# Kernel tuning notes

Hardware: AMD Instinct MI355X
Metric: run time of the kernel (lower is better)

## Reference

```python
import jax, jax.numpy as jnp
import numpy as np

N_NODES = 50000
N_EDGES = 1600000
D = 64  # per-node feature dim for h1 and h2


def setup_inputs() -> dict:
    key = jax.random.key(0)
    ks = jax.random.split(key, 8)
    h1 = jax.random.normal(ks[0], (N_NODES, D), dtype=jnp.float32)
    h2 = jax.random.normal(ks[1], (N_NODES, D), dtype=jnp.float32)
    src = jax.random.randint(ks[2], (N_EDGES,), 0, N_NODES)
    dst = jax.random.randint(ks[3], (N_EDGES,), 0, N_NODES)
    # MLP params: layer_sizes = [256, 128, 128, 1]
    def glorot(k, fan_in, fan_out):
        lim = (6.0 / (fan_in + fan_out)) ** 0.5
        return jax.random.uniform(k, (fan_in, fan_out), jnp.float32, -lim, lim)
    W0 = glorot(ks[4], 4 * D, 128)
    W1 = glorot(ks[5], 128, 128)
    W2 = glorot(ks[6], 128, 1)
    b0 = jnp.zeros((128,), jnp.float32)
    b1 = jnp.zeros((128,), jnp.float32)
    b2 = jnp.zeros((1,), jnp.float32)
    return {"h1": h1, "h2": h2, "src": src, "dst": dst,
            "W0": W0, "b0": b0, "W1": W1, "b1": b1, "W2": W2, "b2": b2}


def reference(h1, h2, src, dst, W0, b0, W1, b1, W2, b2):
    # Edge-wise gather of src/dst node features, concat -> MLP (eval mode: dropout=identity).
    h = jnp.concatenate([h1[src], h1[dst], h2[src], h2[dst]], axis=1)  # [E, 4D]
    h = h @ W0 + b0
    h = jax.nn.relu(h) @ W1 + b1
    h = jax.nn.relu(h) @ W2 + b2
    return h  # [E, out_features]
```

## Files before the change

### kernel.cpp

```cpp
#include <hip/hip_runtime.h>
#include <hip/hip_bf16.h>
#include <stdint.h>


typedef __attribute__((ext_vector_type(8))) __bf16 bf16x8;
typedef __attribute__((ext_vector_type(4))) __bf16 bf16x4;
typedef __attribute__((ext_vector_type(4))) float  floatx4;

__device__ inline floatx4 mfma16x16x32(bf16x8 a, bf16x8 b, floatx4 c) {
  return __builtin_amdgcn_mfma_f32_16x16x32_bf16(a, b, c, 0, 0, 0);
}

__device__ inline void bar_lds() {
  asm volatile("s_waitcnt lgkmcnt(0)" ::: "memory");
  __builtin_amdgcn_s_barrier();
}

__global__ void cvt_w_kernel(const float* __restrict__ W0, const float* __restrict__ W1,
                             __bf16* __restrict__ W1T, __bf16* __restrict__ W0uT,
                             __bf16* __restrict__ W0wT) {
  const int t = blockIdx.x * 256 + threadIdx.x;
  if (t < 16384) {
    const int n = t >> 7, k = t & 127;
    W1T[t] = (__bf16)W1[k * 128 + n];
  } else if (t < 32768) {
    const int t2 = t - 16384;
    const int n = t2 >> 7, k2 = t2 & 127;
    const int row = (k2 < 64) ? k2 : 64 + k2;
    W0uT[t2] = (__bf16)W0[row * 128 + n];
  } else {
    const int t3 = t - 32768;
    const int n = t3 >> 7, k2 = t3 & 127;
    const int row = (k2 < 64) ? 64 + k2 : 128 + k2;
    W0wT[t3] = (__bf16)W0[row * 128 + n];
  }
}

__global__ __launch_bounds__(256, 2)
void node_uw_kernel(const float* __restrict__ h1, const float* __restrict__ h2,
                    const __bf16* __restrict__ W0uT, const __bf16* __restrict__ W0wT,
                    const float* __restrict__ b0,
                    __bf16* __restrict__ uTab, __bf16* __restrict__ wTab, int nNodes) {
  __shared__ char sN[64 * 256];
  const int tid = threadIdx.x;
  const int base = blockIdx.x * 64;

  {
    const int r = tid >> 2, q = tid & 3;
    const int node = base + r;
    const int swz = (r & 7) << 4;
#pragma unroll
    for (int ii = 0; ii < 4; ++ii) {
      const int c = q * 4 + ii;
      bf16x8 v;
      if (node < nNodes) {
        const float* sp = (c < 8) ? (h1 + (size_t)node * 64 + c * 8)
                                  : (h2 + (size_t)node * 64 + (c - 8) * 8);
        const float4 x = reinterpret_cast<const float4*>(sp)[0];
        const float4 y = reinterpret_cast<const float4*>(sp)[1];
        v[0] = (__bf16)x.x; v[1] = (__bf16)x.y; v[2] = (__bf16)x.z; v[3] = (__bf16)x.w;
        v[4] = (__bf16)y.x; v[5] = (__bf16)y.y; v[6] = (__bf16)y.z; v[7] = (__bf16)y.w;
      } else {
#pragma unroll
        for (int k = 0; k < 8; ++k) v[k] = (__bf16)0.f;
      }
      *reinterpret_cast<bf16x8*>(sN + r * 256 + ((c * 16) ^ swz)) = v;
    }
  }
  __syncthreads();

  const int lane = tid & 63;
  const int l15 = lane & 15;
  const int hi = lane >> 4;
  const int hi16 = hi * 16;
  const int wvU = __builtin_amdgcn_readfirstlane(tid >> 6);

  float b0c[2][4];
#pragma unroll
  for (int nt = 0; nt < 2; ++nt)
#pragma unroll
    for (int r = 0; r < 4; ++r) b0c[nt][r] = b0[wvU * 32 + nt * 16 + hi * 4 + r];

#pragma unroll
  for (int pass = 0; pass < 2; ++pass) {
    const __bf16* Wt = pass ? W0wT : W0uT;
    __bf16* Tab = pass ? wTab : uTab;
    const bf16x8* wp = reinterpret_cast<const bf16x8*>(Wt);
    bf16x8 wf[4][2];
#pragma unroll
    for (int kk = 0; kk < 4; ++kk) {
      wf[kk][0] = wp[(wvU * 32 + l15) * 16 + kk * 4 + hi];
      wf[kk][1] = wp[(wvU * 32 + 16 + l15) * 16 + kk * 4 + hi];
    }
    floatx4 acc[4][2];
#pragma unroll
    for (int mt = 0; mt < 4; ++mt) { acc[mt][0] = (floatx4)0.f; acc[mt][1] = (floatx4)0.f; }
#pragma unroll
    for (int kk = 0; kk < 4; ++kk) {
#pragma unroll
      for (int mt = 0; mt < 4; ++mt) {
        const int row = mt * 16 + l15;
        const bf16x8 a = *reinterpret_cast<const bf16x8*>(
            sN + row * 256 + ((kk * 64 + hi16) ^ ((row & 7) << 4)));
        acc[mt][0] = mfma16x16x32(wf[kk][0], a, acc[mt][0]);
        acc[mt][1] = mfma16x16x32(wf[kk][1], a, acc[mt][1]);
      }
    }
#pragma unroll
    for (int mt = 0; mt < 4; ++mt) {
      const int node = base + mt * 16 + l15;
      if (node < nNodes) {
#pragma unroll
        for (int nt = 0; nt < 2; ++nt) {
          bf16x4 pk;
#pragma unroll
          for (int r = 0; r < 4; ++r) {
            const float v = acc[mt][nt][r] + (pass ? 0.f : b0c[nt][r]);
            pk[r] = (__bf16)v;
          }
          *reinterpret_cast<bf16x4*>(Tab + (size_t)node * 128 + wvU * 32 + nt * 16 +
                                     hi * 4) = pk;
        }
      }
    }
  }
}

__global__ __launch_bounds__(256, 2)
void edge_uw_kernel(const __bf16* __restrict__ uTab, const __bf16* __restrict__ wTab,
                    const int* __restrict__ srcI, const int* __restrict__ dstI,
                    const __bf16* __restrict__ W1T, const float* __restrict__ b1,
                    const float* __restrict__ W2, const float* __restrict__ b2,
                    float* __restrict__ out, int E, int nTiles) {
  __shared__ char sUW[2 * 64 * 512];
  __shared__ char sH[64 * 256];

  const int tid = threadIdx.x;
  const int lane = tid & 63;
  const int l15 = lane & 15;
  const int hi = lane >> 4;
  const int hi16 = hi * 16;
  const int wvU = __builtin_amdgcn_readfirstlane(tid >> 6);
  const int wv16 = wvU * 16;
  const int wvByte = wvU * 8192;

  const int lhalf = lane >> 5;
  const int p31 = lane & 31;
  const int half = (p31 >> 4) & 1;
  const int* gIdxTab = half ? dstI : srcI;
  const __bf16* gTab = half ? wTab : uTab;

  bf16x8 w1f[4][2];
  const bf16x8* w1p = reinterpret_cast<const bf16x8*>(W1T);
#pragma unroll
  for (int kk = 0; kk < 4; ++kk) {
    w1f[kk][0] = w1p[(wvU * 32 + l15) * 16 + kk * 4 + hi];
    w1f[kk][1] = w1p[(wvU * 32 + 16 + l15) * 16 + kk * 4 + hi];
  }
  float b1c[2][4], w2c[2][4];
#pragma unroll
  for (int nt = 0; nt < 2; ++nt)
#pragma unroll
    for (int r = 0; r < 4; ++r) {
      const int n = wvU * 32 + nt * 16 + hi * 4 + r;
      b1c[nt][r] = b1[n];
      w2c[nt][r] = W2[n];
    }
  const float b2v = b2[0];

  const int tstride = gridDim.x;

  auto loadIdx = [&](int (&d)[8], int tt2) {
    const bool valid = tt2 < nTiles;
#pragma unroll
    for (int i = 0; i < 8; ++i) {
      const int eLoc = wv16 + i * 2 + lhalf;
      const int ge = tt2 * 64 + eLoc;
      d[i] = (valid && ge < E) ? gIdxTab[ge] : 0;
    }
  };

  auto issueGather = [&](int nb, const int (&idx8)[8]) {
#pragma unroll
    for (int i = 0; i < 8; ++i) {
      const int eLoc = wv16 + i * 2 + lhalf;
      const int wc = (p31 & 8) | ((p31 & 7) ^ (eLoc & 7));
      const __bf16* g = gTab + (size_t)idx8[i] * 128 + (wc & 15) * 8;
      char* l = sUW + nb * 32768 + wvByte + i * 1024;
      __builtin_amdgcn_global_load_lds(
          (const __attribute__((address_space(1))) void*)g,
          (__attribute__((address_space(3))) void*)l, 16, 0, 0);
    }
  };

  const int tile0 = blockIdx.x;
  int idxA[8], idxB[8];
  loadIdx(idxA, tile0);
  issueGather(0, idxA);
  loadIdx(idxB, tile0 + tstride);
  int cur = 0;

  for (int tt = tile0; tt < nTiles; tt += tstride) {
    __syncthreads();

    if (tt + tstride < nTiles) issueGather(cur ^ 1, idxB);
    loadIdx(idxA, tt + 2 * tstride);

    const char* sUWc = sUW + cur * 32768;

    {
      const int aR = wv16 + (lane >> 2);
      const int acq = lane & 3;
      const int aswz = (aR & 7) << 4;
      const char* rowU = sUWc + aR * 512;
      char* rowH = sH + aR * 256;
#pragma unroll
      for (int ii = 0; ii < 4; ++ii) {
        const int c = acq * 4 + ii;
        const int off = (c * 16) ^ aswz;
        const bf16x8 uu = *reinterpret_cast<const bf16x8*>(rowU + off);
        const bf16x8 ww = *reinterpret_cast<const bf16x8*>(rowU + 256 + off);
        bf16x8 hh;
#pragma unroll
        for (int k = 0; k < 8; ++k)
          hh[k] = (__bf16)fmaxf((float)uu[k] + (float)ww[k], 0.0f);
        *reinterpret_cast<bf16x8*>(rowH + off) = hh;
      }
    }
    bar_lds();

    floatx4 acc2T[4][2];
#pragma unroll
    for (int mt = 0; mt < 4; ++mt) { acc2T[mt][0] = (floatx4)0.f; acc2T[mt][1] = (floatx4)0.f; }
#pragma unroll
    for (int kk = 0; kk < 4; ++kk) {
#pragma unroll
      for (int mt = 0; mt < 4; ++mt) {
        const int row = mt * 16 + l15;
        const bf16x8 a = *reinterpret_cast<const bf16x8*>(
            sH + row * 256 + ((kk * 64 + hi16) ^ ((row & 7) << 4)));
        acc2T[mt][0] = mfma16x16x32(w1f[kk][0], a, acc2T[mt][0]);
        acc2T[mt][1] = mfma16x16x32(w1f[kk][1], a, acc2T[mt][1]);
      }
    }

    float* sRedF = (float*)sUWc;
#pragma unroll
    for (int mt = 0; mt < 4; ++mt) {
      float pp = 0.f;
#pragma unroll
      for (int nt = 0; nt < 2; ++nt)
#pragma unroll
        for (int r = 0; r < 4; ++r)
          pp += fmaxf(acc2T[mt][nt][r] + b1c[nt][r], 0.0f) * w2c[nt][r];
      pp += __shfl_xor(pp, 16);
      pp += __shfl_xor(pp, 32);
      if (lane < 16) sRedF[wvU * 64 + mt * 16 + l15] = pp;
    }
    bar_lds();

    if (tid < 64) {
      const int ge = tt * 64 + tid;
      if (ge < E) {
        out[ge] = sRedF[tid] + sRedF[64 + tid] + sRedF[128 + tid] +
                  sRedF[192 + tid] + b2v;
      }
    }

#pragma unroll
    for (int i = 0; i < 8; ++i) idxB[i] = idxA[i];
    cur ^= 1;
  }
}

__global__ void edge_mlp_fallback(const float* __restrict__ h1, const float* __restrict__ h2,
                                  const int* __restrict__ src, const int* __restrict__ dst,
                                  const float* __restrict__ W0, const float* __restrict__ b0,
                                  const float* __restrict__ W1, const float* __restrict__ b1,
                                  const float* __restrict__ W2, const float* __restrict__ b2,
                                  float* __restrict__ out, int E) {
  __shared__ float sa[256];
  __shared__ float sh[128];
  __shared__ float sr[128];
  const int e = blockIdx.x;
  if (e >= E) return;
  const int t = threadIdx.x;
  const int is = src[e], id = dst[e];
  if (t < 64) { sa[t] = h1[is * 64 + t]; sa[128 + t] = h2[is * 64 + t]; }
  else { const int u = t - 64; sa[64 + u] = h1[id * 64 + u]; sa[192 + u] = h2[id * 64 + u]; }
  __syncthreads();
  float a0 = b0[t];
  for (int k = 0; k < 256; ++k) a0 += sa[k] * W0[k * 128 + t];
  sh[t] = fmaxf(a0, 0.f);
  __syncthreads();
  float a1 = b1[t];
  for (int k = 0; k < 128; ++k) a1 += sh[k] * W1[k * 128 + t];
  sr[t] = fmaxf(a1, 0.f) * W2[t];
  __syncthreads();
  if (t == 0) {
    float s = b2[0];
    for (int k = 0; k < 128; ++k) s += sr[k];
    out[e] = s;
  }
}

extern "C" void kernel_launch(void* const* d_in, const int* in_sizes, int n_in,
                              void* d_out, int out_size, void* d_ws, size_t ws_size,
                              hipStream_t stream) {
  const float* h1 = (const float*)d_in[0];
  const float* h2 = (const float*)d_in[1];
  const int* src = (const int*)d_in[2];
  const int* dst = (const int*)d_in[3];
  const float* W0 = (const float*)d_in[4];
  const float* b0 = (const float*)d_in[5];
  const float* W1 = (const float*)d_in[6];
  const float* b1 = (const float*)d_in[7];
  const float* W2 = (const float*)d_in[8];
  const float* b2 = (const float*)d_in[9];
  float* out = (float*)d_out;

  const int D = 64;
  const int nNodes = in_sizes[0] / D;
  const int E = in_sizes[2];

  char* ws = (char*)d_ws;
  __bf16* W1T = (__bf16*)(ws);
  __bf16* W0uT = (__bf16*)(ws + 32768);
  __bf16* W0wT = (__bf16*)(ws + 65536);
  const size_t tabBytes = (size_t)nNodes * 128 * sizeof(__bf16);
  __bf16* uTab = (__bf16*)(ws + 98304);
  __bf16* wTab = (__bf16*)(ws + 98304 + tabBytes);
  const bool useFast = ws_size >= 98304 + 2 * tabBytes;

  if (!useFast) {
    edge_mlp_fallback<<<dim3(E), dim3(128), 0, stream>>>(
        h1, h2, src, dst, W0, b0, W1, b1, W2, b2, out, E);
    return;
  }

  cvt_w_kernel<<<dim3(192), dim3(256), 0, stream>>>(W0, W1, W1T, W0uT, W0wT);
  node_uw_kernel<<<dim3((nNodes + 63) / 64), dim3(256), 0, stream>>>(
      h1, h2, W0uT, W0wT, b0, uTab, wTab, nNodes);

  const int nTiles = (E + 63) / 64;
  const int grid = nTiles < 1024 ? nTiles : 1024;
  edge_uw_kernel<<<dim3(grid), dim3(256), 0, stream>>>(
      uTab, wTab, src, dst, W1T, b1, W2, b2, out, E, nTiles);
}
```

Before: 168.1 us.

## Split edge tile across 8 waves with 2x4 M/N wave grid

The edge kernel now runs 512 threads per block, with 8 waves arranged as 2 row-groups by 4 column-groups over each 64-edge tile. Each wave gathers half as many rows, holds half as many MFMA accumulators, and the cross-wave reduction is stored interleaved so one float4 read produces each output. The grid is halved to 512 blocks to keep total waves roughly constant. The aim is more waves in flight per tile to hide gather latency. The cost is more wave-level synchronisation per tile and W1 fragments being duplicated across the two row-group waves.

```diff
diff --git a/kernel.cpp b/kernel.cpp
--- a/kernel.cpp
+++ b/kernel.cpp
@@ -126,7 +126,7 @@
   }
 }
 
-__global__ __launch_bounds__(256, 2)
+__global__ __launch_bounds__(512, 2)
 void edge_uw_kernel(const __bf16* __restrict__ uTab, const __bf16* __restrict__ wTab,
                     const int* __restrict__ srcI, const int* __restrict__ dstI,
                     const __bf16* __restrict__ W1T, const float* __restrict__ b1,
@@ -141,8 +141,9 @@
   const int hi = lane >> 4;
   const int hi16 = hi * 16;
   const int wvU = __builtin_amdgcn_readfirstlane(tid >> 6);
-  const int wv16 = wvU * 16;
-  const int wvByte = wvU * 8192;
+  const int wm = wvU >> 2;
+  const int wn = wvU & 3;
+  const int wvByte = wvU * 4096;
 
   const int lhalf = lane >> 5;
   const int p31 = lane & 31;
@@ -154,15 +155,15 @@
   const bf16x8* w1p = reinterpret_cast<const bf16x8*>(W1T);
 #pragma unroll
   for (int kk = 0; kk < 4; ++kk) {
-    w1f[kk][0] = w1p[(wvU * 32 + l15) * 16 + kk * 4 + hi];
-    w1f[kk][1] = w1p[(wvU * 32 + 16 + l15) * 16 + kk * 4 + hi];
+    w1f[kk][0] = w1p[(wn * 32 + l15) * 16 + kk * 4 + hi];
+    w1f[kk][1] = w1p[(wn * 32 + 16 + l15) * 16 + kk * 4 + hi];
   }
   float b1c[2][4], w2c[2][4];
 #pragma unroll
   for (int nt = 0; nt < 2; ++nt)
 #pragma unroll
     for (int r = 0; r < 4; ++r) {
-      const int n = wvU * 32 + nt * 16 + hi * 4 + r;
+      const int n = wn * 32 + nt * 16 + hi * 4 + r;
       b1c[nt][r] = b1[n];
       w2c[nt][r] = W2[n];
     }
@@ -170,22 +171,22 @@
 
   const int tstride = gridDim.x;
 
-  auto loadIdx = [&](int (&d)[8], int tt2) {
+  auto loadIdx = [&](int (&d)[4], int tt2) {
     const bool valid = tt2 < nTiles;
 #pragma unroll
-    for (int i = 0; i < 8; ++i) {
-      const int eLoc = wv16 + i * 2 + lhalf;
+    for (int i = 0; i < 4; ++i) {
+      const int eLoc = wvU * 8 + i * 2 + lhalf;
       const int ge = tt2 * 64 + eLoc;
       d[i] = (valid && ge < E) ? gIdxTab[ge] : 0;
     }
   };
 
-  auto issueGather = [&](int nb, const int (&idx8)[8]) {
-#pragma unroll
-    for (int i = 0; i < 8; ++i) {
-      const int eLoc = wv16 + i * 2 + lhalf;
+  auto issueGather = [&](int nb, const int (&idx4)[4]) {
+#pragma unroll
+    for (int i = 0; i < 4; ++i) {
+      const int eLoc = wvU * 8 + i * 2 + lhalf;
       const int wc = (p31 & 8) | ((p31 & 7) ^ (eLoc & 7));
-      const __bf16* g = gTab + (size_t)idx8[i] * 128 + (wc & 15) * 8;
+      const __bf16* g = gTab + (size_t)idx4[i] * 128 + wc * 8;
       char* l = sUW + nb * 32768 + wvByte + i * 1024;
       __builtin_amdgcn_global_load_lds(
           (const __attribute__((address_space(1))) void*)g,
@@ -194,7 +195,7 @@
   };
 
   const int tile0 = blockIdx.x;
-  int idxA[8], idxB[8];
+  int idxA[4], idxB[4];
   loadIdx(idxA, tile0);
   issueGather(0, idxA);
   loadIdx(idxB, tile0 + tstride);
@@ -209,14 +210,14 @@
     const char* sUWc = sUW + cur * 32768;
 
     {
-      const int aR = wv16 + (lane >> 2);
-      const int acq = lane & 3;
+      const int aR = tid >> 3;
+      const int q = tid & 7;
       const int aswz = (aR & 7) << 4;
       const char* rowU = sUWc + aR * 512;
       char* rowH = sH + aR * 256;
 #pragma unroll
-      for (int ii = 0; ii < 4; ++ii) {
-        const int c = acq * 4 + ii;
+      for (int ii = 0; ii < 2; ++ii) {
+        const int c = q * 2 + ii;
         const int off = (c * 16) ^ aswz;
         const bf16x8 uu = *reinterpret_cast<const bf16x8*>(rowU + off);
         const bf16x8 ww = *reinterpret_cast<const bf16x8*>(rowU + 256 + off);
@@ -229,14 +230,14 @@
     }
     bar_lds();
 
-    floatx4 acc2T[4][2];
-#pragma unroll
-    for (int mt = 0; mt < 4; ++mt) { acc2T[mt][0] = (floatx4)0.f; acc2T[mt][1] = (floatx4)0.f; }
+    floatx4 acc2T[2][2];
+#pragma unroll
+    for (int mt = 0; mt < 2; ++mt) { acc2T[mt][0] = (floatx4)0.f; acc2T[mt][1] = (floatx4)0.f; }
 #pragma unroll
     for (int kk = 0; kk < 4; ++kk) {
 #pragma unroll
-      for (int mt = 0; mt < 4; ++mt) {
-        const int row = mt * 16 + l15;
+      for (int mt = 0; mt < 2; ++mt) {
+        const int row = wm * 32 + mt * 16 + l15;
         const bf16x8 a = *reinterpret_cast<const bf16x8*>(
             sH + row * 256 + ((kk * 64 + hi16) ^ ((row & 7) << 4)));
         acc2T[mt][0] = mfma16x16x32(w1f[kk][0], a, acc2T[mt][0]);
@@ -246,7 +247,7 @@
 
     float* sRedF = (float*)sUWc;
 #pragma unroll
-    for (int mt = 0; mt < 4; ++mt) {
+    for (int mt = 0; mt < 2; ++mt) {
       float pp = 0.f;
 #pragma unroll
       for (int nt = 0; nt < 2; ++nt)
@@ -255,20 +256,20 @@
           pp += fmaxf(acc2T[mt][nt][r] + b1c[nt][r], 0.0f) * w2c[nt][r];
       pp += __shfl_xor(pp, 16);
       pp += __shfl_xor(pp, 32);
-      if (lane < 16) sRedF[wvU * 64 + mt * 16 + l15] = pp;
+      if (lane < 16) sRedF[(wm * 32 + mt * 16 + l15) * 4 + wn] = pp;
     }
     bar_lds();
 
     if (tid < 64) {
       const int ge = tt * 64 + tid;
       if (ge < E) {
-        out[ge] = sRedF[tid] + sRedF[64 + tid] + sRedF[128 + tid] +
-                  sRedF[192 + tid] + b2v;
-      }
-    }
-
-#pragma unroll
-    for (int i = 0; i < 8; ++i) idxB[i] = idxA[i];
+        const float4 v = reinterpret_cast<const float4*>(sRedF)[tid];
+        out[ge] = v.x + v.y + v.z + v.w + b2v;
+      }
+    }
+
+#pragma unroll
+    for (int i = 0; i < 4; ++i) idxB[i] = idxA[i];
     cur ^= 1;
   }
 }
@@ -343,7 +344,7 @@
       h1, h2, W0uT, W0wT, b0, uTab, wTab, nNodes);
 
   const int nTiles = (E + 63) / 64;
-  const int grid = nTiles < 1024 ? nTiles : 1024;
-  edge_uw_kernel<<<dim3(grid), dim3(256), 0, stream>>>(
+  const int grid = nTiles < 512 ? nTiles : 512;
+  edge_uw_kernel<<<dim3(grid), dim3(512), 0, stream>>>(
       uTab, wTab, src, dst, W1T, b1, W2, b2, out, E, nTiles);
 }
```

After: 151.7 us. 9.7% less time.
